# Kernel optimization log

Measured on AMD Instinct MI355X. Metric: run time of the kernel, lower is better.

## Reference

```python
import jax, jax.numpy as jnp
import numpy as np

B = 4          # batch size
NP = 20000     # points per batch element (equal-length ragged segments)
C = 256        # decode_seg_dim / KPConv in=out channels
NN = 16        # k-NN neighbors
K = 15         # KPConv kernel points
NCLS = 17      # num_classes
GS_H, GS_W = 32, 128   # patch_num
KP_EXTENT = 1.2
RADIUS = 0.6
BN_EPS = 1e-5


def setup_inputs() -> dict:
    key = jax.random.key(0)
    ks = jax.random.split(key, 10)
    x = jax.random.normal(ks[0], (B, GS_H * GS_W, C), jnp.float32)
    skip = jax.random.normal(ks[1], (B, 64, 64, 1024), jnp.float32)
    px = jax.random.uniform(ks[2], (B * NP,), jnp.float32, -1.0, 1.0)
    py = jax.random.uniform(ks[3], (B * NP,), jnp.float32, -1.0, 1.0)
    pxyz = jax.random.normal(ks[4], (B * NP, 3), jnp.float32) * 0.3
    pknn = jax.random.randint(ks[5], (B * NP, NN), 0, NP, jnp.int32)  # per-batch local indices
    num_points = jnp.full((B,), NP, jnp.int32)
    kernel_points = jax.random.normal(ks[6], (K, 3), jnp.float32) * (RADIUS * 0.5)
    kp_weights = jax.random.normal(ks[7], (K, C, C), jnp.float32) * (1.0 / np.sqrt(K * C))
    bn_gamma = jnp.ones((C,), jnp.float32)
    bn_beta = jnp.zeros((C,), jnp.float32)
    head_w = jax.random.normal(ks[8], (NCLS, C), jnp.float32) * 0.05
    head_b = jnp.zeros((NCLS,), jnp.float32)
    return dict(x=x, skip=skip, px=px, py=py, pxyz=pxyz, pknn=pknn,
                num_points=num_points, kernel_points=kernel_points,
                kp_weights=kp_weights, bn_gamma=bn_gamma, bn_beta=bn_beta,
                head_w=head_w, head_b=head_b)


def _grid_sample_border(img, px, py):
    # img: [C,H,W]; px,py in [-1,1]; bilinear, align_corners=False, border padding.
    _, H, W = img.shape
    ix = jnp.clip(((px + 1.0) * W - 1.0) * 0.5, 0.0, W - 1.0)
    iy = jnp.clip(((py + 1.0) * H - 1.0) * 0.5, 0.0, H - 1.0)
    x0 = jnp.floor(ix); y0 = jnp.floor(iy)
    wx = ix - x0; wy = iy - y0
    x0i = x0.astype(jnp.int32); y0i = y0.astype(jnp.int32)
    x1i = jnp.minimum(x0i + 1, W - 1); y1i = jnp.minimum(y0i + 1, H - 1)
    g = lambda yi, xi: img[:, yi, xi]  # [C, N]
    out = (g(y0i, x0i) * (1 - wx) * (1 - wy) + g(y0i, x1i) * wx * (1 - wy)
           + g(y1i, x0i) * (1 - wx) * wy + g(y1i, x1i) * wx * wy)
    return out.T  # [N, C]


def _kpconv(points, pknn, feats, kernel_points, kp_weights):
    # Rigid KPConv, linear influence, sum aggregation.
    neighbors = points[pknn] - points[:, None, :]                      # [N,NN,3]
    diff = neighbors[:, :, None, :] - kernel_points[None, None]        # [N,NN,K,3]
    sq_d = jnp.sum(diff * diff, axis=-1)                               # [N,NN,K]
    w = jnp.maximum(1.0 - jnp.sqrt(sq_d) / KP_EXTENT, 0.0)             # [N,NN,K]
    nx = feats[pknn]                                                   # [N,NN,Cin]
    wf = jnp.einsum('nak,nac->nkc', w, nx)                             # [N,K,Cin]
    return jnp.einsum('nkc,kcd->nd', wf, kp_weights)                   # [N,Cout]


def _forward(x, px, py, pxyz, pknn, kernel_points, kp_weights,
             bn_gamma, bn_beta, head_w, head_b):
    b = x.shape[0]
    n_per = px.shape[0] // b
    # rearrange 'b (h w) c -> b c h w'
    xi = x.reshape(b, GS_H, GS_W, -1).transpose(0, 3, 1, 2)
    feats = jax.vmap(_grid_sample_border)(xi, px.reshape(b, n_per), py.reshape(b, n_per))  # [B,N,C]
    kp = lambda p, nn, f: _kpconv(p, nn, f, kernel_points, kp_weights)
    out = jax.vmap(kp)(pxyz.reshape(b, n_per, 3), pknn.reshape(b, n_per, NN), feats)       # [B,N,C]
    out = out.reshape(b * n_per, -1)
    # BatchNorm2d (training mode: batch stats over all points), then ReLU, then 1x1 conv head
    mean = out.mean(axis=0)
    var = out.var(axis=0)
    h = jnp.maximum(bn_gamma * (out - mean) * jax.lax.rsqrt(var + BN_EPS) + bn_beta, 0.0)
    logits = h @ head_w.T + head_b                                     # [B*N, NCLS]
    return logits[:, :, None, None]


def reference(x, skip, px, py, pxyz, pknn, num_points, kernel_points,
              kp_weights, bn_gamma, bn_beta, head_w, head_b):
    # Note: MyHead computes up_conv_block(x, skip) but only returns masks3d,
    # which does not depend on it -> dead code, omitted (skip is unused).
    del skip, num_points
    return _forward(x, px, py, pxyz, pknn, kernel_points, kp_weights,
                    bn_gamma, bn_beta, head_w, head_b)
```

## Files before the change

### kernel.cpp

```cpp
#include <hip/hip_runtime.h>

#define NPTS 80000
#define NPER 20000
#define CDIM 256
#define NNB  16
#define NKP  15
#define NCLS 17
#define GSH  32
#define GSW  128

typedef __bf16 bf16x8 __attribute__((ext_vector_type(8)));
typedef float  f32x4  __attribute__((ext_vector_type(4)));

__device__ __forceinline__ unsigned short f2bf(float f){
    unsigned int u = __float_as_uint(f);
    u = u + 0x7FFFu + ((u >> 16) & 1u);
    return (unsigned short)(u >> 16);
}
__device__ __forceinline__ unsigned int pack2(float a, float b){
    return (unsigned int)f2bf(a) | ((unsigned int)f2bf(b) << 16);
}

#define GLD_LDS16(gsrc, ldst) \
    __builtin_amdgcn_global_load_lds((const __attribute__((address_space(1))) unsigned int*)(gsrc), \
                                     (__attribute__((address_space(3))) unsigned int*)(ldst), 16, 0, 0)

#define WS_KPWT   40960000
#define WS_OUT    42926080
#define WS_STATS  124846080
#define WS_NEED   124848128

#define B7_BASE 917504

__global__ void zero_stats_kernel(float* stats){ stats[threadIdx.x] = 0.f; }

__global__ __launch_bounds__(256) void gs_kernel(
    const float* __restrict__ x, const float* __restrict__ px,
    const float* __restrict__ py, unsigned short* __restrict__ feats)
{
    int gid = blockIdx.x * 256 + threadIdx.x;
    int n = gid >> 6;
    if (n >= NPTS) return;
    int c0 = (gid & 63) << 2;
    int b = n / NPER;
    float ix = fminf(fmaxf(((px[n] + 1.f) * (float)GSW - 1.f) * 0.5f, 0.f), (float)(GSW - 1));
    float iy = fminf(fmaxf(((py[n] + 1.f) * (float)GSH - 1.f) * 0.5f, 0.f), (float)(GSH - 1));
    float x0f = floorf(ix), y0f = floorf(iy);
    float wx = ix - x0f, wy = iy - y0f;
    int x0 = (int)x0f, y0 = (int)y0f;
    int x1 = min(x0 + 1, GSW - 1), y1 = min(y0 + 1, GSH - 1);
    const float* base = x + (size_t)b * (GSH * GSW * CDIM);
    float4 v00 = *(const float4*)(base + ((size_t)(y0 * GSW + x0)) * CDIM + c0);
    float4 v01 = *(const float4*)(base + ((size_t)(y0 * GSW + x1)) * CDIM + c0);
    float4 v10 = *(const float4*)(base + ((size_t)(y1 * GSW + x0)) * CDIM + c0);
    float4 v11 = *(const float4*)(base + ((size_t)(y1 * GSW + x1)) * CDIM + c0);
    float w00 = (1.f - wx) * (1.f - wy), w01 = wx * (1.f - wy);
    float w10 = (1.f - wx) * wy,         w11 = wx * wy;
    float r0 = v00.x * w00 + v01.x * w01 + v10.x * w10 + v11.x * w11;
    float r1 = v00.y * w00 + v01.y * w01 + v10.y * w10 + v11.y * w11;
    float r2 = v00.z * w00 + v01.z * w01 + v10.z * w10 + v11.z * w11;
    float r3 = v00.w * w00 + v01.w * w01 + v10.w * w10 + v11.w * w11;
    ushort4 o; o.x = f2bf(r0); o.y = f2bf(r1); o.z = f2bf(r2); o.w = f2bf(r3);
    *(ushort4*)(feats + (size_t)n * CDIM + c0) = o;
}

__global__ __launch_bounds__(256) void wt_kernel(
    const float* __restrict__ kpw, unsigned short* __restrict__ kpwS)
{
    int gid = blockIdx.x * 256 + threadIdx.x;
    int k = gid >> 16;
    int c = (gid >> 8) & 255;
    int d = gid & 255;
    unsigned short v = f2bf(kpw[gid]);
    int pair = k >> 1, kwin = k & 1, chunk = c >> 4, cl = c & 15;
    int kap = kwin * 16 + cl;
    int q = kap >> 3, j = kap & 7;
    int m = d & 15, ctg = d >> 4;
    int idx;
    if (pair < 7) idx = (chunk * 7 + pair) * 8192 + (ctg * 64 + q * 16 + m) * 8 + j;
    else          idx = B7_BASE + chunk * 4096 + (ctg * 32 + q * 16 + m) * 8 + j;
    kpwS[idx] = v;
}

__global__ __launch_bounds__(256, 2) void kpconv_kernel(
    const unsigned short* __restrict__ feats,
    const unsigned short* __restrict__ kpwS,
    const int*   __restrict__ pknn,
    const float* __restrict__ pxyz,
    const float* __restrict__ kp_pts,
    float* __restrict__ outbuf,
    float* __restrict__ stats)
{
    __shared__ unsigned short s_f[16384];
    __shared__ unsigned short s_wf2[16384];

    int tid = threadIdx.x;
    int n0  = blockIdx.x * 64;
    int wv = tid >> 6, lane = tid & 63, m = lane & 15, q = lane >> 4;

    int fb[8];
    {
        int pl = lane >> 5, a = (lane >> 1) & 15, half = lane & 1;
#pragma unroll
        for (int i = 0; i < 8; i++){
            int n = n0 + wv * 16 + 2 * i + pl;
            int b = n / NPER;
            fb[i] = (b * NPER + pknn[(size_t)n * NNB + a]) * CDIM + half * 8;
        }
    }
#pragma unroll
    for (int i = 0; i < 8; i++)
        GLD_LDS16(feats + (size_t)fb[i], (char*)s_f + wv * 8192 + i * 1024);

    unsigned int wfrag[16][2];
    {
        int km = (m < 15) ? m : 14;
        float kx = kp_pts[km * 3 + 0], ky = kp_pts[km * 3 + 1], kz = kp_pts[km * 3 + 2];
        int4 nb[16];
#pragma unroll
        for (int p = 0; p < 16; p++){
            int n = n0 + wv * 16 + p;
            nb[p] = *(const int4*)&pknn[(size_t)n * NNB + 4 * q];
        }
#pragma unroll
        for (int p = 0; p < 16; p++){
            int n = n0 + wv * 16 + p;
            int b = n / NPER;
            float cx = pxyz[n * 3 + 0], cy = pxyz[n * 3 + 1], cz = pxyz[n * 3 + 2];
            int gi[4] = { nb[p].x, nb[p].y, nb[p].z, nb[p].w };
            float w[4];
#pragma unroll
            for (int e = 0; e < 4; e++){
                int g = b * NPER + gi[e];
                float ex = pxyz[g * 3 + 0] - cx - kx;
                float ey = pxyz[g * 3 + 1] - cy - ky;
                float ez = pxyz[g * 3 + 2] - cz - kz;
                float d = sqrtf(ex * ex + ey * ey + ez * ez);
                w[e] = (m < 15) ? fmaxf(1.f - d * (1.f / 1.2f), 0.f) : 0.f;
            }
            wfrag[p][0] = pack2(w[0], w[1]);
            wfrag[p][1] = pack2(w[2], w[3]);
        }
    }

    f32x4 acc[4][4];
#pragma unroll
    for (int i = 0; i < 4; i++)
#pragma unroll
        for (int j = 0; j < 4; j++){ acc[i][j][0]=0.f; acc[i][j][1]=0.f; acc[i][j][2]=0.f; acc[i][j][3]=0.f; }

    unsigned trb;
    {
        unsigned sbase = (unsigned)(size_t)(__attribute__((address_space(3))) unsigned short*)s_f;
        trb = sbase + (unsigned)(wv * 8192 + m * 8 + q * 128);
    }
    int xr = (m & 7) << 3;

#define WF_MFMA_PACK(p) { \
        union { uint4 u; bf16x8 v; } Af, Bw; \
        Af.u = make_uint4(tr[p].x, tr[p].y, 0u, 0u); \
        Bw.u = make_uint4(wfrag[p][0], wfrag[p][1], 0u, 0u); \
        f32x4 dz; dz[0]=0.f; dz[1]=0.f; dz[2]=0.f; dz[3]=0.f; \
        f32x4 d = __builtin_amdgcn_mfma_f32_16x16x32_bf16(Af.v, Bw.v, dz, 0, 0, 0); \
        uint2 o; o.x = pack2(d[0], d[1]); o.y = pack2(d[2], d[3]); \
        *(uint2*)&s_wf2[(((wv * 16 + (p)) * 256 + m * 16 + 4 * q)) ^ (((p) & 7) << 3)] = o; }

#define GEMM_WINDOW(P, BREG) { \
        bf16x8 A[4]; \
        _Pragma("unroll") \
        for (int rt = 0; rt < 4; rt++) \
            A[rt] = *(const bf16x8*)&s_wf2[(((16 * rt + m) * 256 + (2 * (P) + (q >> 1)) * 16 + (q & 1) * 8)) ^ xr]; \
        __builtin_amdgcn_s_setprio(1); \
        _Pragma("unroll") \
        for (int ct = 0; ct < 4; ct++) \
            _Pragma("unroll") \
            for (int rt = 0; rt < 4; rt++) \
                acc[rt][ct] = __builtin_amdgcn_mfma_f32_16x16x32_bf16(A[rt], BREG[ct], acc[rt][ct], 0, 0, 0); \
        __builtin_amdgcn_s_setprio(0); }

#define PREFETCH_B(Pn, BREG) { \
        if ((Pn) < 7){ \
            const unsigned short* bb = kpwS + (c * 7 + (Pn)) * 8192 + (q * 16 + m) * 8; \
            _Pragma("unroll") \
            for (int ct = 0; ct < 4; ct++) BREG[ct] = *(const bf16x8*)(bb + (wv * 4 + ct) * 512); \
        } else { \
            const unsigned short* bb = kpwS + B7_BASE + c * 4096 + ((q & 1) * 16 + m) * 8; \
            _Pragma("unroll") \
            for (int ct = 0; ct < 4; ct++) BREG[ct] = *(const bf16x8*)(bb + (wv * 4 + ct) * 256); \
        } }

    for (int c = 0; c < 16; c++){
        asm volatile("s_waitcnt vmcnt(0)" ::: "memory");

        uint2 tr[16];
#pragma unroll
        for (int p = 0; p < 8; p++)
            asm volatile("ds_read_b64_tr_b16 %0, %1 offset:%2"
                         : "=v"(tr[p]) : "v"(trb), "i"(p * 512));
#pragma unroll
        for (int p = 8; p < 16; p++)
            asm volatile("ds_read_b64_tr_b16 %0, %1 offset:%2"
                         : "=v"(tr[p]) : "v"(trb), "i"(p * 512));

        asm volatile("s_waitcnt lgkmcnt(8)" ::: "memory");
        __builtin_amdgcn_sched_barrier(0);
#pragma unroll
        for (int p = 0; p < 8; p++) WF_MFMA_PACK(p)

        asm volatile("s_waitcnt lgkmcnt(8)" ::: "memory");
        __builtin_amdgcn_sched_barrier(0);
#pragma unroll
        for (int p = 8; p < 16; p++) WF_MFMA_PACK(p)

        bf16x8 B0[4], B1[4];
        PREFETCH_B(0, B0)
        PREFETCH_B(1, B1)

        asm volatile("s_waitcnt lgkmcnt(0)\ns_barrier" ::: "memory");

        GEMM_WINDOW(0, B0)  PREFETCH_B(2, B0)
        GEMM_WINDOW(1, B1)  PREFETCH_B(3, B1)
        GEMM_WINDOW(2, B0)  PREFETCH_B(4, B0)
        GEMM_WINDOW(3, B1)  PREFETCH_B(5, B1)
        GEMM_WINDOW(4, B0)  PREFETCH_B(6, B0)
        GEMM_WINDOW(5, B1)  PREFETCH_B(7, B1)
        if (c < 15){
#pragma unroll
            for (int i = 0; i < 8; i++)
                GLD_LDS16(feats + (size_t)(fb[i] + (c + 1) * 16), (char*)s_f + wv * 8192 + i * 1024);
        }
        GEMM_WINDOW(6, B0)
        GEMM_WINDOW(7, B1)

        asm volatile("s_waitcnt lgkmcnt(0)\ns_barrier" ::: "memory");
    }
#undef WF_MFMA_PACK
#undef GEMM_WINDOW
#undef PREFETCH_B

#pragma unroll
    for (int rt = 0; rt < 4; rt++)
#pragma unroll
        for (int ct = 0; ct < 4; ct++)
#pragma unroll
            for (int r = 0; r < 4; r++){
                int prow = 16 * rt + 4 * q + r;
                int d = wv * 64 + ct * 16 + m;
                outbuf[(size_t)(n0 + prow) * CDIM + d] = acc[rt][ct][r];
            }
#pragma unroll
    for (int ct = 0; ct < 4; ct++){
        float s1 = 0.f, s2 = 0.f;
#pragma unroll
        for (int rt = 0; rt < 4; rt++)
#pragma unroll
            for (int r = 0; r < 4; r++){
                float v = acc[rt][ct][r];
                s1 += v; s2 += v * v;
            }
        s1 += __shfl_xor(s1, 16); s1 += __shfl_xor(s1, 32);
        s2 += __shfl_xor(s2, 16); s2 += __shfl_xor(s2, 32);
        if (q == 0){
            int d = wv * 64 + ct * 16 + m;
            atomicAdd(&stats[d], s1);
            atomicAdd(&stats[256 + d], s2);
        }
    }
}

__global__ __launch_bounds__(256) void head_kernel(
    const float* __restrict__ outbuf, const float* __restrict__ stats,
    const float* __restrict__ gamma,  const float* __restrict__ beta,
    const float* __restrict__ hw,     const float* __restrict__ hb,
    float* __restrict__ logits)
{
    __shared__ float s_h[16][256];
    int tid = threadIdx.x;
    int n0 = blockIdx.x * 16;
    int pt = tid >> 4, cgr = tid & 15;
    {
        int n = n0 + pt;
        const float invN = 1.f / (float)NPTS;
#pragma unroll
        for (int j = 0; j < 16; j += 4){
            int c = cgr * 16 + j;
            float4 v  = *(const float4*)(outbuf + (size_t)n * CDIM + c);
            float4 su = *(const float4*)(stats + c);
            float4 sq = *(const float4*)(stats + 256 + c);
            float4 ga = *(const float4*)(gamma + c);
            float4 be = *(const float4*)(beta + c);
            float mean, var;
            mean = su.x * invN; var = sq.x * invN - mean * mean;
            s_h[pt][c + 0] = fmaxf(ga.x * (v.x - mean) * rsqrtf(var + 1e-5f) + be.x, 0.f);
            mean = su.y * invN; var = sq.y * invN - mean * mean;
            s_h[pt][c + 1] = fmaxf(ga.y * (v.y - mean) * rsqrtf(var + 1e-5f) + be.y, 0.f);
            mean = su.z * invN; var = sq.z * invN - mean * mean;
            s_h[pt][c + 2] = fmaxf(ga.z * (v.z - mean) * rsqrtf(var + 1e-5f) + be.z, 0.f);
            mean = su.w * invN; var = sq.w * invN - mean * mean;
            s_h[pt][c + 3] = fmaxf(ga.w * (v.w - mean) * rsqrtf(var + 1e-5f) + be.w, 0.f);
        }
    }
    __syncthreads();
    for (int idx = tid; idx < 16 * NCLS; idx += 256){
        int pt2 = idx / NCLS, cls = idx - pt2 * NCLS;
        float acc = hb[cls];
#pragma unroll 8
        for (int c = 0; c < CDIM; c += 4){
            float4 h4 = *(const float4*)&s_h[pt2][c];
            float4 w4 = *(const float4*)(hw + (size_t)cls * CDIM + c);
            acc = fmaf(h4.x, w4.x, fmaf(h4.y, w4.y, fmaf(h4.z, w4.z, fmaf(h4.w, w4.w, acc))));
        }
        logits[(size_t)(n0 + pt2) * NCLS + cls] = acc;
    }
}

extern "C" void kernel_launch(void* const* d_in, const int* in_sizes, int n_in,
                              void* d_out, int out_size, void* d_ws, size_t ws_size,
                              hipStream_t stream)
{
    (void)in_sizes; (void)n_in; (void)out_size;
    if (ws_size < (size_t)WS_NEED) return;

    const float* x      = (const float*)d_in[0];
    const float* px     = (const float*)d_in[2];
    const float* py     = (const float*)d_in[3];
    const float* pxyz   = (const float*)d_in[4];
    const int*   pknn   = (const int*)  d_in[5];
    const float* kp_pts = (const float*)d_in[7];
    const float* kpw    = (const float*)d_in[8];
    const float* gamma  = (const float*)d_in[9];
    const float* beta   = (const float*)d_in[10];
    const float* hw     = (const float*)d_in[11];
    const float* hb     = (const float*)d_in[12];
    float* logits = (float*)d_out;

    char* ws = (char*)d_ws;
    unsigned short* feats = (unsigned short*)(ws);
    unsigned short* kpwS  = (unsigned short*)(ws + WS_KPWT);
    float* outbuf = (float*)(ws + WS_OUT);
    float* stats  = (float*)(ws + WS_STATS);

    hipLaunchKernelGGL(zero_stats_kernel, dim3(1),     dim3(512), 0, stream, stats);
    hipLaunchKernelGGL(gs_kernel,         dim3(20000), dim3(256), 0, stream, x, px, py, feats);
    hipLaunchKernelGGL(wt_kernel,         dim3(3840),  dim3(256), 0, stream, kpw, kpwS);
    hipLaunchKernelGGL(kpconv_kernel,     dim3(1250),  dim3(256), 0, stream,
                       feats, kpwS, pknn, pxyz, kp_pts, outbuf, stats);
    hipLaunchKernelGGL(head_kernel,       dim3(5000),  dim3(256), 0, stream,
                       outbuf, stats, gamma, beta, hw, hb, logits);
}
```

Measured before the change: 670.9 us.

## Replace direct-to-LDS gather with register double-buffered prefetch two chunks ahead

Neighbour-feature gathers now load into registers (two alternating register sets) instead of using global_load_lds, and are issued two chunks ahead, then written to LDS at the start of each chunk. This drops the full vmcnt(0) wait at the top of every chunk and gives gather latency more time to hide behind the MFMA work. The cost is 64 extra VGPRs for the staging buffers, which can lower occupancy or cause spills, plus explicit LDS store instructions.

```diff
diff --git a/kernel.cpp b/kernel.cpp
--- a/kernel.cpp
+++ b/kernel.cpp
@@ -20,10 +20,6 @@
 __device__ __forceinline__ unsigned int pack2(float a, float b){
     return (unsigned int)f2bf(a) | ((unsigned int)f2bf(b) << 16);
 }
-
-#define GLD_LDS16(gsrc, ldst) \
-    __builtin_amdgcn_global_load_lds((const __attribute__((address_space(1))) unsigned int*)(gsrc), \
-                                     (__attribute__((address_space(3))) unsigned int*)(ldst), 16, 0, 0)
 
 #define WS_KPWT   40960000
 #define WS_OUT    42926080
@@ -108,9 +104,19 @@
             fb[i] = (b * NPER + pknn[(size_t)n * NNB + a]) * CDIM + half * 8;
         }
     }
-#pragma unroll
-    for (int i = 0; i < 8; i++)
-        GLD_LDS16(feats + (size_t)fb[i], (char*)s_f + wv * 8192 + i * 1024);
+
+    uint4 rgA[8], rgB[8];
+#define GATHER_ISSUE(cn, R) { \
+        _Pragma("unroll") \
+        for (int i = 0; i < 8; i++) \
+            R[i] = *(const uint4*)(feats + (size_t)(fb[i] + (cn) * 16)); }
+#define STAGE_WRITE(R) { \
+        _Pragma("unroll") \
+        for (int i = 0; i < 8; i++) \
+            *(uint4*)((char*)s_f + wv * 8192 + i * 1024 + lane * 16) = R[i]; }
+
+    GATHER_ISSUE(0, rgA)
+    GATHER_ISSUE(1, rgB)
 
     unsigned int wfrag[16][2];
     {
@@ -189,54 +195,54 @@
             for (int ct = 0; ct < 4; ct++) BREG[ct] = *(const bf16x8*)(bb + (wv * 4 + ct) * 256); \
         } }
 
-    for (int c = 0; c < 16; c++){
-        asm volatile("s_waitcnt vmcnt(0)" ::: "memory");
-
-        uint2 tr[16];
-#pragma unroll
-        for (int p = 0; p < 8; p++)
-            asm volatile("ds_read_b64_tr_b16 %0, %1 offset:%2"
-                         : "=v"(tr[p]) : "v"(trb), "i"(p * 512));
-#pragma unroll
-        for (int p = 8; p < 16; p++)
-            asm volatile("ds_read_b64_tr_b16 %0, %1 offset:%2"
-                         : "=v"(tr[p]) : "v"(trb), "i"(p * 512));
-
-        asm volatile("s_waitcnt lgkmcnt(8)" ::: "memory");
-        __builtin_amdgcn_sched_barrier(0);
-#pragma unroll
-        for (int p = 0; p < 8; p++) WF_MFMA_PACK(p)
-
-        asm volatile("s_waitcnt lgkmcnt(8)" ::: "memory");
-        __builtin_amdgcn_sched_barrier(0);
-#pragma unroll
-        for (int p = 8; p < 16; p++) WF_MFMA_PACK(p)
-
-        bf16x8 B0[4], B1[4];
-        PREFETCH_B(0, B0)
-        PREFETCH_B(1, B1)
-
-        asm volatile("s_waitcnt lgkmcnt(0)\ns_barrier" ::: "memory");
-
-        GEMM_WINDOW(0, B0)  PREFETCH_B(2, B0)
-        GEMM_WINDOW(1, B1)  PREFETCH_B(3, B1)
-        GEMM_WINDOW(2, B0)  PREFETCH_B(4, B0)
-        GEMM_WINDOW(3, B1)  PREFETCH_B(5, B1)
-        GEMM_WINDOW(4, B0)  PREFETCH_B(6, B0)
-        GEMM_WINDOW(5, B1)  PREFETCH_B(7, B1)
-        if (c < 15){
-#pragma unroll
-            for (int i = 0; i < 8; i++)
-                GLD_LDS16(feats + (size_t)(fb[i] + (c + 1) * 16), (char*)s_f + wv * 8192 + i * 1024);
-        }
-        GEMM_WINDOW(6, B0)
-        GEMM_WINDOW(7, B1)
-
-        asm volatile("s_waitcnt lgkmcnt(0)\ns_barrier" ::: "memory");
-    }
+#define CHUNK_BODY(CEXPR, R, DOISS) { \
+        const int c = (CEXPR); \
+        STAGE_WRITE(R) \
+        asm volatile("" ::: "memory"); \
+        __builtin_amdgcn_sched_barrier(0); \
+        uint2 tr[16]; \
+        _Pragma("unroll") \
+        for (int p = 0; p < 8; p++) \
+            asm volatile("ds_read_b64_tr_b16 %0, %1 offset:%2" \
+                         : "=v"(tr[p]) : "v"(trb), "i"(p * 512)); \
+        _Pragma("unroll") \
+        for (int p = 8; p < 16; p++) \
+            asm volatile("ds_read_b64_tr_b16 %0, %1 offset:%2" \
+                         : "=v"(tr[p]) : "v"(trb), "i"(p * 512)); \
+        asm volatile("s_waitcnt lgkmcnt(8)" ::: "memory"); \
+        __builtin_amdgcn_sched_barrier(0); \
+        _Pragma("unroll") \
+        for (int p = 0; p < 8; p++) WF_MFMA_PACK(p) \
+        asm volatile("s_waitcnt lgkmcnt(8)" ::: "memory"); \
+        __builtin_amdgcn_sched_barrier(0); \
+        _Pragma("unroll") \
+        for (int p = 8; p < 16; p++) WF_MFMA_PACK(p) \
+        bf16x8 B0[4], B1[4]; \
+        PREFETCH_B(0, B0) \
+        PREFETCH_B(1, B1) \
+        asm volatile("s_waitcnt lgkmcnt(0)\ns_barrier" ::: "memory"); \
+        GEMM_WINDOW(0, B0)  PREFETCH_B(2, B0) \
+        GEMM_WINDOW(1, B1)  PREFETCH_B(3, B1) \
+        GEMM_WINDOW(2, B0)  PREFETCH_B(4, B0) \
+        GEMM_WINDOW(3, B1)  PREFETCH_B(5, B1) \
+        GEMM_WINDOW(4, B0)  PREFETCH_B(6, B0) \
+        GEMM_WINDOW(5, B1)  PREFETCH_B(7, B1) \
+        if (DOISS) GATHER_ISSUE((c) + 2, R) \
+        GEMM_WINDOW(6, B0) \
+        GEMM_WINDOW(7, B1) \
+        asm volatile("s_waitcnt lgkmcnt(0)\ns_barrier" ::: "memory"); \
+    }
+
+    for (int cc = 0; cc < 16; cc += 2){
+        CHUNK_BODY(cc,     rgA, (cc < 14))
+        CHUNK_BODY(cc + 1, rgB, (cc < 13))
+    }
+#undef CHUNK_BODY
 #undef WF_MFMA_PACK
 #undef GEMM_WINDOW
 #undef PREFETCH_B
+#undef GATHER_ISSUE
+#undef STAGE_WRITE
 
 #pragma unroll
     for (int rt = 0; rt < 4; rt++)
```

After: 1.186 ms. +76.8%, slower.

## Split weighted-feature staging into two halves to halve LDS buffer

Applied to the files above, without the earlier changes.

The KPConv main loop now builds the weighted-feature tile in two halves per channel chunk, each half written to a smaller s_wf2 buffer half the previous size, followed by four GEMM windows per half. The full 16 MFMA packs are still computed each half, but only the lanes whose m half matches store results. This cuts LDS use and register pressure (tr[16] becomes tr[4], and one B register set instead of two), which may allow more blocks per CU. The cost is doubled transposed-read and MFMA work for the packing step, extra barriers per chunk, and less prefetch overlap.

```diff
diff --git a/kernel.cpp b/kernel.cpp
--- a/kernel.cpp
+++ b/kernel.cpp
@@ -92,7 +92,7 @@
     float* __restrict__ stats)
 {
     __shared__ unsigned short s_f[16384];
-    __shared__ unsigned short s_wf2[16384];
+    __shared__ unsigned short s_wf2[8192];
 
     int tid = threadIdx.x;
     int n0  = blockIdx.x * 64;
@@ -156,20 +156,21 @@
     }
     int xr = (m & 7) << 3;
 
-#define WF_MFMA_PACK(p) { \
+#define WF_MFMA_PACK(p, i, h) { \
         union { uint4 u; bf16x8 v; } Af, Bw; \
-        Af.u = make_uint4(tr[p].x, tr[p].y, 0u, 0u); \
+        Af.u = make_uint4(tr[i].x, tr[i].y, 0u, 0u); \
         Bw.u = make_uint4(wfrag[p][0], wfrag[p][1], 0u, 0u); \
         f32x4 dz; dz[0]=0.f; dz[1]=0.f; dz[2]=0.f; dz[3]=0.f; \
         f32x4 d = __builtin_amdgcn_mfma_f32_16x16x32_bf16(Af.v, Bw.v, dz, 0, 0, 0); \
-        uint2 o; o.x = pack2(d[0], d[1]); o.y = pack2(d[2], d[3]); \
-        *(uint2*)&s_wf2[(((wv * 16 + (p)) * 256 + m * 16 + 4 * q)) ^ (((p) & 7) << 3)] = o; }
-
-#define GEMM_WINDOW(P, BREG) { \
+        if ((m >> 3) == (h)) { \
+            uint2 o; o.x = pack2(d[0], d[1]); o.y = pack2(d[2], d[3]); \
+            *(uint2*)&s_wf2[(((wv * 16 + (p)) * 128 + (m & 7) * 16 + 4 * q)) ^ (((p) & 7) << 3)] = o; } }
+
+#define GEMM_WINDOW_L(Ph, BREG) { \
         bf16x8 A[4]; \
         _Pragma("unroll") \
         for (int rt = 0; rt < 4; rt++) \
-            A[rt] = *(const bf16x8*)&s_wf2[(((16 * rt + m) * 256 + (2 * (P) + (q >> 1)) * 16 + (q & 1) * 8)) ^ xr]; \
+            A[rt] = *(const bf16x8*)&s_wf2[(((16 * rt + m) * 128 + (2 * (Ph) + (q >> 1)) * 16 + (q & 1) * 8)) ^ xr]; \
         __builtin_amdgcn_s_setprio(1); \
         _Pragma("unroll") \
         for (int ct = 0; ct < 4; ct++) \
@@ -192,50 +193,44 @@
     for (int c = 0; c < 16; c++){
         asm volatile("s_waitcnt vmcnt(0)" ::: "memory");
 
-        uint2 tr[16];
-#pragma unroll
-        for (int p = 0; p < 8; p++)
-            asm volatile("ds_read_b64_tr_b16 %0, %1 offset:%2"
-                         : "=v"(tr[p]) : "v"(trb), "i"(p * 512));
-#pragma unroll
-        for (int p = 8; p < 16; p++)
-            asm volatile("ds_read_b64_tr_b16 %0, %1 offset:%2"
-                         : "=v"(tr[p]) : "v"(trb), "i"(p * 512));
-
-        asm volatile("s_waitcnt lgkmcnt(8)" ::: "memory");
-        __builtin_amdgcn_sched_barrier(0);
-#pragma unroll
-        for (int p = 0; p < 8; p++) WF_MFMA_PACK(p)
-
-        asm volatile("s_waitcnt lgkmcnt(8)" ::: "memory");
-        __builtin_amdgcn_sched_barrier(0);
-#pragma unroll
-        for (int p = 8; p < 16; p++) WF_MFMA_PACK(p)
-
-        bf16x8 B0[4], B1[4];
-        PREFETCH_B(0, B0)
-        PREFETCH_B(1, B1)
-
-        asm volatile("s_waitcnt lgkmcnt(0)\ns_barrier" ::: "memory");
-
-        GEMM_WINDOW(0, B0)  PREFETCH_B(2, B0)
-        GEMM_WINDOW(1, B1)  PREFETCH_B(3, B1)
-        GEMM_WINDOW(2, B0)  PREFETCH_B(4, B0)
-        GEMM_WINDOW(3, B1)  PREFETCH_B(5, B1)
-        GEMM_WINDOW(4, B0)  PREFETCH_B(6, B0)
-        GEMM_WINDOW(5, B1)  PREFETCH_B(7, B1)
-        if (c < 15){
-#pragma unroll
-            for (int i = 0; i < 8; i++)
-                GLD_LDS16(feats + (size_t)(fb[i] + (c + 1) * 16), (char*)s_f + wv * 8192 + i * 1024);
-        }
-        GEMM_WINDOW(6, B0)
-        GEMM_WINDOW(7, B1)
-
-        asm volatile("s_waitcnt lgkmcnt(0)\ns_barrier" ::: "memory");
+#pragma unroll
+        for (int h = 0; h < 2; h++){
+#pragma unroll
+            for (int g = 0; g < 4; g++){
+                uint2 tr[4];
+#pragma unroll
+                for (int i = 0; i < 4; i++)
+                    asm volatile("ds_read_b64_tr_b16 %0, %1 offset:%2"
+                                 : "=v"(tr[i]) : "v"(trb), "i"((4 * g + i) * 512));
+                asm volatile("s_waitcnt lgkmcnt(0)" ::: "memory");
+                __builtin_amdgcn_sched_barrier(0);
+#pragma unroll
+                for (int i = 0; i < 4; i++) WF_MFMA_PACK(4 * g + i, i, h)
+            }
+
+            bf16x8 B[4];
+            PREFETCH_B(4 * h + 0, B)
+
+            asm volatile("s_waitcnt lgkmcnt(0)\ns_barrier" ::: "memory");
+
+            GEMM_WINDOW_L(0, B)
+            PREFETCH_B(4 * h + 1, B)
+            GEMM_WINDOW_L(1, B)
+            PREFETCH_B(4 * h + 2, B)
+            GEMM_WINDOW_L(2, B)
+            PREFETCH_B(4 * h + 3, B)
+            if (h == 1 && c < 15){
+#pragma unroll
+                for (int i = 0; i < 8; i++)
+                    GLD_LDS16(feats + (size_t)(fb[i] + (c + 1) * 16), (char*)s_f + wv * 8192 + i * 1024);
+            }
+            GEMM_WINDOW_L(3, B)
+
+            asm volatile("s_waitcnt lgkmcnt(0)\ns_barrier" ::: "memory");
+        }
     }
 #undef WF_MFMA_PACK
-#undef GEMM_WINDOW
+#undef GEMM_WINDOW_L
 #undef PREFETCH_B
 
 #pragma unroll
```

Result: slower. 723.0 us (+7.8%).

## Halve kpconv point tile to 32 and stage two channel chunks per load

Applied to the files above, without the earlier changes.

The kpconv kernel now handles 32 points per block instead of 64 and launches twice as many blocks. Each feature staging load now brings in two 16-channel chunks, so the channel loop makes 8 passes of 2 sub-chunks instead of 16 passes. The change also shrinks the accumulator registers and the LDS scratch, and hoists the batch row offset out of the loop. The goal is more blocks to fill the machine and fewer global-to-LDS reload rounds. In exchange, each weight tile fetched from kpwS is reused across fewer points, so total weight traffic from L2 doubles.

```diff
diff --git a/kernel.cpp b/kernel.cpp
--- a/kernel.cpp
+++ b/kernel.cpp
@@ -92,46 +92,45 @@
     float* __restrict__ stats)
 {
     __shared__ unsigned short s_f[16384];
-    __shared__ unsigned short s_wf2[16384];
+    __shared__ unsigned short s_wf2[8192];
 
     int tid = threadIdx.x;
-    int n0  = blockIdx.x * 64;
+    int n0  = blockIdx.x * 32;
     int wv = tid >> 6, lane = tid & 63, m = lane & 15, q = lane >> 4;
+    const int brow = (n0 / NPER) * NPER;
 
     int fb[8];
     {
-        int pl = lane >> 5, a = (lane >> 1) & 15, half = lane & 1;
-#pragma unroll
-        for (int i = 0; i < 8; i++){
-            int n = n0 + wv * 16 + 2 * i + pl;
-            int b = n / NPER;
-            fb[i] = (b * NPER + pknn[(size_t)n * NNB + a]) * CDIM + half * 8;
-        }
-    }
-#pragma unroll
-    for (int i = 0; i < 8; i++)
-        GLD_LDS16(feats + (size_t)fb[i], (char*)s_f + wv * 8192 + i * 1024);
-
-    unsigned int wfrag[16][2];
+        int e = lane >> 5, a = (lane >> 1) & 15, h = lane & 1;
+#pragma unroll
+        for (int p = 0; p < 8; p++){
+            int n = n0 + wv * 8 + p;
+            fb[p] = (brow + pknn[(size_t)n * NNB + a]) * CDIM + e * 16 + h * 8;
+        }
+    }
+#pragma unroll
+    for (int p = 0; p < 8; p++)
+        GLD_LDS16(feats + (size_t)fb[p], (char*)s_f + wv * 8192 + p * 1024);
+
+    unsigned int wfrag[8][2];
     {
         int km = (m < 15) ? m : 14;
         float kx = kp_pts[km * 3 + 0], ky = kp_pts[km * 3 + 1], kz = kp_pts[km * 3 + 2];
-        int4 nb[16];
-#pragma unroll
-        for (int p = 0; p < 16; p++){
-            int n = n0 + wv * 16 + p;
+        int4 nb[8];
+#pragma unroll
+        for (int p = 0; p < 8; p++){
+            int n = n0 + wv * 8 + p;
             nb[p] = *(const int4*)&pknn[(size_t)n * NNB + 4 * q];
         }
 #pragma unroll
-        for (int p = 0; p < 16; p++){
-            int n = n0 + wv * 16 + p;
-            int b = n / NPER;
+        for (int p = 0; p < 8; p++){
+            int n = n0 + wv * 8 + p;
             float cx = pxyz[n * 3 + 0], cy = pxyz[n * 3 + 1], cz = pxyz[n * 3 + 2];
             int gi[4] = { nb[p].x, nb[p].y, nb[p].z, nb[p].w };
             float w[4];
 #pragma unroll
             for (int e = 0; e < 4; e++){
-                int g = b * NPER + gi[e];
+                int g = brow + gi[e];
                 float ex = pxyz[g * 3 + 0] - cx - kx;
                 float ey = pxyz[g * 3 + 1] - cy - ky;
                 float ez = pxyz[g * 3 + 2] - cz - kz;
@@ -143,9 +142,9 @@
         }
     }
 
-    f32x4 acc[4][4];
-#pragma unroll
-    for (int i = 0; i < 4; i++)
+    f32x4 acc[2][4];
+#pragma unroll
+    for (int i = 0; i < 2; i++)
 #pragma unroll
         for (int j = 0; j < 4; j++){ acc[i][j][0]=0.f; acc[i][j][1]=0.f; acc[i][j][2]=0.f; acc[i][j][3]=0.f; }
 
@@ -163,83 +162,84 @@
         f32x4 dz; dz[0]=0.f; dz[1]=0.f; dz[2]=0.f; dz[3]=0.f; \
         f32x4 d = __builtin_amdgcn_mfma_f32_16x16x32_bf16(Af.v, Bw.v, dz, 0, 0, 0); \
         uint2 o; o.x = pack2(d[0], d[1]); o.y = pack2(d[2], d[3]); \
-        *(uint2*)&s_wf2[(((wv * 16 + (p)) * 256 + m * 16 + 4 * q)) ^ (((p) & 7) << 3)] = o; }
+        *(uint2*)&s_wf2[(((wv * 8 + (p)) * 256 + m * 16 + 4 * q)) ^ (((p) & 7) << 3)] = o; }
 
 #define GEMM_WINDOW(P, BREG) { \
-        bf16x8 A[4]; \
+        bf16x8 A[2]; \
         _Pragma("unroll") \
-        for (int rt = 0; rt < 4; rt++) \
+        for (int rt = 0; rt < 2; rt++) \
             A[rt] = *(const bf16x8*)&s_wf2[(((16 * rt + m) * 256 + (2 * (P) + (q >> 1)) * 16 + (q & 1) * 8)) ^ xr]; \
         __builtin_amdgcn_s_setprio(1); \
         _Pragma("unroll") \
         for (int ct = 0; ct < 4; ct++) \
             _Pragma("unroll") \
-            for (int rt = 0; rt < 4; rt++) \
+            for (int rt = 0; rt < 2; rt++) \
                 acc[rt][ct] = __builtin_amdgcn_mfma_f32_16x16x32_bf16(A[rt], BREG[ct], acc[rt][ct], 0, 0, 0); \
         __builtin_amdgcn_s_setprio(0); }
 
-#define PREFETCH_B(Pn, BREG) { \
+#define PREFETCH_B(CC, Pn, BREG) { \
         if ((Pn) < 7){ \
-            const unsigned short* bb = kpwS + (c * 7 + (Pn)) * 8192 + (q * 16 + m) * 8; \
+            const unsigned short* bb = kpwS + ((CC) * 7 + (Pn)) * 8192 + (q * 16 + m) * 8; \
             _Pragma("unroll") \
             for (int ct = 0; ct < 4; ct++) BREG[ct] = *(const bf16x8*)(bb + (wv * 4 + ct) * 512); \
         } else { \
-            const unsigned short* bb = kpwS + B7_BASE + c * 4096 + ((q & 1) * 16 + m) * 8; \
+            const unsigned short* bb = kpwS + B7_BASE + (CC) * 4096 + ((q & 1) * 16 + m) * 8; \
             _Pragma("unroll") \
             for (int ct = 0; ct < 4; ct++) BREG[ct] = *(const bf16x8*)(bb + (wv * 4 + ct) * 256); \
         } }
 
-    for (int c = 0; c < 16; c++){
+    for (int cp = 0; cp < 8; cp++){
         asm volatile("s_waitcnt vmcnt(0)" ::: "memory");
 
-        uint2 tr[16];
-#pragma unroll
-        for (int p = 0; p < 8; p++)
-            asm volatile("ds_read_b64_tr_b16 %0, %1 offset:%2"
-                         : "=v"(tr[p]) : "v"(trb), "i"(p * 512));
-#pragma unroll
-        for (int p = 8; p < 16; p++)
-            asm volatile("ds_read_b64_tr_b16 %0, %1 offset:%2"
-                         : "=v"(tr[p]) : "v"(trb), "i"(p * 512));
-
-        asm volatile("s_waitcnt lgkmcnt(8)" ::: "memory");
-        __builtin_amdgcn_sched_barrier(0);
-#pragma unroll
-        for (int p = 0; p < 8; p++) WF_MFMA_PACK(p)
-
-        asm volatile("s_waitcnt lgkmcnt(8)" ::: "memory");
-        __builtin_amdgcn_sched_barrier(0);
-#pragma unroll
-        for (int p = 8; p < 16; p++) WF_MFMA_PACK(p)
-
-        bf16x8 B0[4], B1[4];
-        PREFETCH_B(0, B0)
-        PREFETCH_B(1, B1)
-
-        asm volatile("s_waitcnt lgkmcnt(0)\ns_barrier" ::: "memory");
-
-        GEMM_WINDOW(0, B0)  PREFETCH_B(2, B0)
-        GEMM_WINDOW(1, B1)  PREFETCH_B(3, B1)
-        GEMM_WINDOW(2, B0)  PREFETCH_B(4, B0)
-        GEMM_WINDOW(3, B1)  PREFETCH_B(5, B1)
-        GEMM_WINDOW(4, B0)  PREFETCH_B(6, B0)
-        GEMM_WINDOW(5, B1)  PREFETCH_B(7, B1)
-        if (c < 15){
-#pragma unroll
-            for (int i = 0; i < 8; i++)
-                GLD_LDS16(feats + (size_t)(fb[i] + (c + 1) * 16), (char*)s_f + wv * 8192 + i * 1024);
-        }
-        GEMM_WINDOW(6, B0)
-        GEMM_WINDOW(7, B1)
-
-        asm volatile("s_waitcnt lgkmcnt(0)\ns_barrier" ::: "memory");
+#pragma unroll
+        for (int e = 0; e < 2; e++){
+            const int c = 2 * cp + e;
+
+            uint2 tr[8];
+#pragma unroll
+            for (int p = 0; p < 8; p++)
+                asm volatile("ds_read_b64_tr_b16 %0, %1 offset:%2"
+                             : "=v"(tr[p]) : "v"(trb), "i"(p * 1024 + e * 512));
+
+            asm volatile("s_waitcnt lgkmcnt(4)" ::: "memory");
+            __builtin_amdgcn_sched_barrier(0);
+#pragma unroll
+            for (int p = 0; p < 4; p++) WF_MFMA_PACK(p)
+
+            asm volatile("s_waitcnt lgkmcnt(4)" ::: "memory");
+            __builtin_amdgcn_sched_barrier(0);
+#pragma unroll
+            for (int p = 4; p < 8; p++) WF_MFMA_PACK(p)
+
+            bf16x8 B0[4], B1[4];
+            PREFETCH_B(c, 0, B0)
+            PREFETCH_B(c, 1, B1)
+
+            asm volatile("s_waitcnt lgkmcnt(0)\ns_barrier" ::: "memory");
+
+            GEMM_WINDOW(0, B0)  PREFETCH_B(c, 2, B0)
+            GEMM_WINDOW(1, B1)  PREFETCH_B(c, 3, B1)
+            GEMM_WINDOW(2, B0)  PREFETCH_B(c, 4, B0)
+            GEMM_WINDOW(3, B1)  PREFETCH_B(c, 5, B1)
+            GEMM_WINDOW(4, B0)  PREFETCH_B(c, 6, B0)
+            GEMM_WINDOW(5, B1)  PREFETCH_B(c, 7, B1)
+            if (e == 1 && cp < 7){
+#pragma unroll
+                for (int p = 0; p < 8; p++)
+                    GLD_LDS16(feats + (size_t)(fb[p] + (cp + 1) * 32), (char*)s_f + wv * 8192 + p * 1024);
+            }
+            GEMM_WINDOW(6, B0)
+            GEMM_WINDOW(7, B1)
+
+            asm volatile("s_waitcnt lgkmcnt(0)\ns_barrier" ::: "memory");
+        }
     }
 #undef WF_MFMA_PACK
 #undef GEMM_WINDOW
 #undef PREFETCH_B
 
 #pragma unroll
-    for (int rt = 0; rt < 4; rt++)
+    for (int rt = 0; rt < 2; rt++)
 #pragma unroll
         for (int ct = 0; ct < 4; ct++)
 #pragma unroll
@@ -252,7 +252,7 @@
     for (int ct = 0; ct < 4; ct++){
         float s1 = 0.f, s2 = 0.f;
 #pragma unroll
-        for (int rt = 0; rt < 4; rt++)
+        for (int rt = 0; rt < 2; rt++)
 #pragma unroll
             for (int r = 0; r < 4; r++){
                 float v = acc[rt][ct][r];
@@ -343,7 +343,7 @@
     hipLaunchKernelGGL(zero_stats_kernel, dim3(1),     dim3(512), 0, stream, stats);
     hipLaunchKernelGGL(gs_kernel,         dim3(20000), dim3(256), 0, stream, x, px, py, feats);
     hipLaunchKernelGGL(wt_kernel,         dim3(3840),  dim3(256), 0, stream, kpw, kpwS);
-    hipLaunchKernelGGL(kpconv_kernel,     dim3(1250),  dim3(256), 0, stream,
+    hipLaunchKernelGGL(kpconv_kernel,     dim3(2500),  dim3(256), 0, stream,
                        feats, kpwS, pknn, pxyz, kp_pts, outbuf, stats);
     hipLaunchKernelGGL(head_kernel,       dim3(5000),  dim3(256), 0, stream,
                        outbuf, stats, gamma, beta, hw, hb, logits);
```

Result: faster. 628.3 us (-6.4%).
